# Kernel optimization log

Hardware: AMD Instinct MI355X
Metric: run time of the kernel (lower is better)

The kernel has to match this reference:

```python
import jax, jax.numpy as jnp
import numpy as np

N_CHANNELS = 1024
N_HEADS = 16
BLOCK_SIZE = 2048
BATCH = 4
SEQ = 2048


def setup_inputs() -> dict:
    key = jax.random.key(0)
    k_x, k_wqkv, k_wproj = jax.random.split(key, 3)
    x = jax.random.normal(k_x, (BATCH, SEQ, N_CHANNELS), dtype=jnp.float32)
    # torch nn.Linear: y = x @ W.T + b, W shape [out, in], init normal(std=0.02)
    W_qkv = jax.random.normal(k_wqkv, (3 * N_CHANNELS, N_CHANNELS), dtype=jnp.float32) * 0.02
    b_qkv = jnp.zeros((3 * N_CHANNELS,), dtype=jnp.float32)
    W_proj = jax.random.normal(k_wproj, (N_CHANNELS, N_CHANNELS), dtype=jnp.float32) * 0.02
    b_proj = jnp.zeros((N_CHANNELS,), dtype=jnp.float32)
    return {"x": x, "W_qkv": W_qkv, "b_qkv": b_qkv, "W_proj": W_proj, "b_proj": b_proj}


def reference(x, W_qkv, b_qkv, W_proj, b_proj):
    bs, n, n_channels = x.shape
    n_heads = N_HEADS
    head_dim = n_channels // n_heads
    scale = head_dim ** (-0.5)

    qkv = x @ W_qkv.T + b_qkv                              # [b, n, 3C]
    qkv = qkv.reshape(bs, n, 3, n_heads, head_dim)
    q, k, v = qkv[:, :, 0], qkv[:, :, 1], qkv[:, :, 2]     # [b, n, h, d]

    logits = jnp.einsum('bthc,bshc->bhts', q, k) * scale   # [b, h, t, s]
    # causal mask: log(tril(ones)) = 0 below diagonal, -inf above
    causal = jnp.tril(jnp.ones((n, n), dtype=bool))
    logits = jnp.where(causal[None, None], logits, -jnp.inf)
    attn = jax.nn.softmax(logits, axis=-1)

    output = jnp.einsum('bhts,bshc->bthc', attn, v)        # [b, t, h, d]
    output = output.reshape(bs, n, n_channels)
    output = output @ W_proj.T + b_proj
    return output
```

## Files before the change

### kernel.cpp

```cpp
#include <hip/hip_runtime.h>
#include <hip/hip_bf16.h>
#include <stdint.h>

#define BATCH 4
#define SEQ   2048
#define NC    1024
#define NH    16
#define HD    64
#define NT    16

typedef __bf16 bf16x8 __attribute__((ext_vector_type(8)));
typedef __bf16 bf16x4 __attribute__((ext_vector_type(4)));
typedef float  f32x4  __attribute__((ext_vector_type(4)));

#define DEV __device__ __forceinline__

DEV unsigned short f2bf(float f) {
    union { float f; unsigned u; } v; v.f = f;
    unsigned r = (v.u + 0x7fffu + ((v.u >> 16) & 1u)) >> 16;
    return (unsigned short)r;
}

DEV float fast_exp2(float x) {
#if __has_builtin(__builtin_amdgcn_exp2f)
    return __builtin_amdgcn_exp2f(x);
#else
    return exp2f(x);
#endif
}

#define GLDS16(gsrc, ldst)                                                           \
    __builtin_amdgcn_global_load_lds(                                                \
        (const __attribute__((address_space(1))) unsigned int*)(gsrc),               \
        (__attribute__((address_space(3))) unsigned int*)(ldst), 16, 0, 0)

__global__ void cvt_kernel(const float* __restrict__ in, unsigned short* __restrict__ out, int n4) {
    int i = blockIdx.x * 256 + threadIdx.x;
    if (i >= n4) return;
    float4 v = reinterpret_cast<const float4*>(in)[i];
    ushort4 o;
    o.x = f2bf(v.x); o.y = f2bf(v.y); o.z = f2bf(v.z); o.w = f2bf(v.w);
    reinterpret_cast<ushort4*>(out)[i] = o;
}

template <bool BF16_OUT>
__global__ __launch_bounds__(256, 2) void gemm_bt_kernel(
    const unsigned short* __restrict__ A,
    const unsigned short* __restrict__ W,
    const float* __restrict__ bias,
    void* __restrict__ Cout,
    int M, int N, int K, int scale_n, float scale)
{
    __shared__ __align__(16) char Alds[128 * 128];
    __shared__ __align__(16) char Blds[128 * 128];

    const int tid = threadIdx.x;
    const int w = tid >> 6, l = tid & 63, g = l >> 4, lr = l & 15;
    const int nt = N >> 7;
    const int mtile = blockIdx.x / nt, ntile = blockIdx.x % nt;
    const int m0 = mtile << 7, n0 = ntile << 7;
    const int wr = (w >> 1) << 6, wc = (w & 1) << 6;

    f32x4 acc[4][4] = {};

    for (int kt = 0; kt < K; kt += 64) {
        if (kt) __syncthreads();
#pragma unroll
        for (int i = 0; i < 4; ++i) {
            const int issue = (i << 2) + w;
            const int row = (issue << 3) + (l >> 3);
            const int chunk = (l & 7) ^ (row & 7);
            GLDS16((const char*)(A + (size_t)(m0 + row) * K + kt) + (chunk << 4),
                   Alds + (issue << 10));
        }
#pragma unroll
        for (int i = 0; i < 4; ++i) {
            const int issue = (i << 2) + w;
            const int row = (issue << 3) + (l >> 3);
            const int chunk = (l & 7) ^ (row & 7);
            GLDS16((const char*)(W + (size_t)(n0 + row) * K + kt) + (chunk << 4),
                   Blds + (issue << 10));
        }
        __syncthreads();

#pragma unroll
        for (int kb = 0; kb < 2; ++kb) {
            bf16x8 af[4], bfr[4];
#pragma unroll
            for (int mf = 0; mf < 4; ++mf) {
                const int row = wr + (mf << 4) + lr;
                const int chunk = ((kb << 2) + g) ^ (row & 7);
                af[mf] = *reinterpret_cast<const bf16x8*>(Alds + row * 128 + (chunk << 4));
            }
#pragma unroll
            for (int nf = 0; nf < 4; ++nf) {
                const int row = wc + (nf << 4) + lr;
                const int chunk = ((kb << 2) + g) ^ (row & 7);
                bfr[nf] = *reinterpret_cast<const bf16x8*>(Blds + row * 128 + (chunk << 4));
            }
#pragma unroll
            for (int mf = 0; mf < 4; ++mf)
#pragma unroll
                for (int nf = 0; nf < 4; ++nf)
                    acc[mf][nf] = __builtin_amdgcn_mfma_f32_16x16x32_bf16(
                        af[mf], bfr[nf], acc[mf][nf], 0, 0, 0);
        }
    }

#pragma unroll
    for (int mf = 0; mf < 4; ++mf) {
#pragma unroll
        for (int nf = 0; nf < 4; ++nf) {
            const int n = n0 + wc + (nf << 4) + lr;
            const float bscale = (n < scale_n) ? scale : 1.0f;
            const float bv = bias[n];
#pragma unroll
            for (int r = 0; r < 4; ++r) {
                const int m = m0 + wr + (mf << 4) + (g << 2) + r;
                float v2 = (acc[mf][nf][r] + bv) * bscale;
                if (BF16_OUT)
                    ((unsigned short*)Cout)[(size_t)m * N + n] = f2bf(v2);
                else
                    ((float*)Cout)[(size_t)m * N + n] = v2;
            }
        }
    }
}

__global__ __launch_bounds__(256, 2) void attn_kernel(
    const unsigned short* __restrict__ qkv,
    unsigned short* __restrict__ ctx)
{
    __shared__ __align__(16) char Klds[2][8192];
    __shared__ __align__(16) char Vt[2][64 * 144];
    __shared__ __align__(16) char Pl[4][32 * 144];

    const int tid = threadIdx.x;
    const int w = tid >> 6, l = tid & 63, g = l >> 4, lr = l & 15;
    const int p = blockIdx.x, h = blockIdx.y, b = blockIdx.z;
    const unsigned short* base = qkv + (size_t)b * SEQ * 3072 + h * 64;
    char* Pw = Pl[w];

    const int vkey0 = (tid >> 5) << 3;
    const int vd0   = (tid & 31) << 1;
    const unsigned short* vbase = base + 2048 + (size_t)vkey0 * 3072 + vd0;

    for (int pass = 0; pass < 2; ++pass) {
        const int qt = pass ? (NT - 1 - p) : p;
        const int q0 = (qt << 7) + (w << 5);
        const int ntiles = (qt + 1) << 1;

        bf16x8 qfr[2][2];
#pragma unroll
        for (int qi = 0; qi < 2; ++qi)
#pragma unroll
            for (int kb = 0; kb < 2; ++kb)
                qfr[qi][kb] = *reinterpret_cast<const bf16x8*>(
                    base + (size_t)(q0 + (qi << 4) + lr) * 3072 + (kb << 5) + (g << 3));

        f32x4 acc[2][4] = {};
        float mrun[2] = {-INFINITY, -INFINITY};
        float lrun[2] = {0.f, 0.f};

        uint32_t vreg[8];

#pragma unroll
        for (int i = 0; i < 8; ++i)
            vreg[i] = *reinterpret_cast<const uint32_t*>(vbase + (size_t)i * 3072);
#pragma unroll
        for (int i = 0; i < 2; ++i) {
            const int issue = (i << 2) + w;
            const int row = (issue << 3) + (l >> 3);
            const int chunk = (l & 7) ^ (row & 7);
            GLDS16((const char*)(base + 1024 + (size_t)row * 3072) + (chunk << 4),
                   Klds[0] + (issue << 10));
        }
        {
            uint4 a, bq;
            a.x = (vreg[0] & 0xffffu) | (vreg[1] << 16);
            a.y = (vreg[2] & 0xffffu) | (vreg[3] << 16);
            a.z = (vreg[4] & 0xffffu) | (vreg[5] << 16);
            a.w = (vreg[6] & 0xffffu) | (vreg[7] << 16);
            bq.x = (vreg[0] >> 16) | (vreg[1] & 0xffff0000u);
            bq.y = (vreg[2] >> 16) | (vreg[3] & 0xffff0000u);
            bq.z = (vreg[4] >> 16) | (vreg[5] & 0xffff0000u);
            bq.w = (vreg[6] >> 16) | (vreg[7] & 0xffff0000u);
            *reinterpret_cast<uint4*>(Vt[0] + vd0 * 144 + vkey0 * 2) = a;
            *reinterpret_cast<uint4*>(Vt[0] + (vd0 + 1) * 144 + vkey0 * 2) = bq;
        }
        __syncthreads();

        for (int t = 0; t < ntiles; ++t) {
            const int cur = t & 1;
            const int kv0 = t << 6;
            const bool pf_ = (t + 1 < ntiles);

            if (pf_) {
                const int kv1 = kv0 + 64;
#pragma unroll
                for (int i = 0; i < 8; ++i)
                    vreg[i] = *reinterpret_cast<const uint32_t*>(
                        vbase + (size_t)(kv1 + i) * 3072);
#pragma unroll
                for (int i = 0; i < 2; ++i) {
                    const int issue = (i << 2) + w;
                    const int row = (issue << 3) + (l >> 3);
                    const int chunk = (l & 7) ^ (row & 7);
                    GLDS16((const char*)(base + 1024 + (size_t)(kv1 + row) * 3072) + (chunk << 4),
                           Klds[cur ^ 1] + (issue << 10));
                }
            }

            if (kv0 <= q0 + 31) {
                f32x4 st[4][2] = {};
#pragma unroll
                for (int kb = 0; kb < 2; ++kb) {
                    bf16x8 kfr[4];
#pragma unroll
                    for (int kf = 0; kf < 4; ++kf) {
                        const int row = (kf << 4) + lr;
                        const int chunk = ((kb << 2) + g) ^ (row & 7);
                        kfr[kf] = *reinterpret_cast<const bf16x8*>(
                            Klds[cur] + row * 128 + (chunk << 4));
                    }
#pragma unroll
                    for (int kf = 0; kf < 4; ++kf)
#pragma unroll
                        for (int qi = 0; qi < 2; ++qi)
                            st[kf][qi] = __builtin_amdgcn_mfma_f32_16x16x32_bf16(
                                kfr[kf], qfr[qi][kb], st[kf][qi], 0, 0, 0);
                }
#pragma unroll
                for (int qi = 0; qi < 2; ++qi) {
                    const int qg = q0 + (qi << 4) + lr;
                    if (kv0 + 63 > qg) {
#pragma unroll
                        for (int kf = 0; kf < 4; ++kf)
#pragma unroll
                            for (int r = 0; r < 4; ++r) {
                                const int key = kv0 + (kf << 4) + (g << 2) + r;
                                if (key > qg) st[kf][qi][r] = -INFINITY;
                            }
                    }
                    float mt = -INFINITY;
#pragma unroll
                    for (int kf = 0; kf < 4; ++kf)
#pragma unroll
                        for (int r = 0; r < 4; ++r) mt = fmaxf(mt, st[kf][qi][r]);
                    mt = fmaxf(mt, __shfl_xor(mt, 16));
                    mt = fmaxf(mt, __shfl_xor(mt, 32));
                    const float mnew = fmaxf(mrun[qi], mt);
                    const float corr = fast_exp2(mrun[qi] - mnew);
                    mrun[qi] = mnew;
                    float rs = 0.f;
#pragma unroll
                    for (int kf = 0; kf < 4; ++kf) {
                        float p0 = fast_exp2(st[kf][qi][0] - mnew);
                        float p1 = fast_exp2(st[kf][qi][1] - mnew);
                        float p2 = fast_exp2(st[kf][qi][2] - mnew);
                        float p3 = fast_exp2(st[kf][qi][3] - mnew);
                        rs += (p0 + p1) + (p2 + p3);
                        bf16x4 pv = {(__bf16)p0, (__bf16)p1, (__bf16)p2, (__bf16)p3};
                        *reinterpret_cast<bf16x4*>(
                            Pw + (qi * 16 + lr) * 144 + (((kf << 4) + (g << 2)) << 1)) = pv;
                    }
                    rs += __shfl_xor(rs, 16);
                    rs += __shfl_xor(rs, 32);
                    lrun[qi] = lrun[qi] * corr + rs;
                    float cr[4];
#pragma unroll
                    for (int r = 0; r < 4; ++r) cr[r] = __shfl(corr, (l & 48) | ((g << 2) + r));
#pragma unroll
                    for (int df = 0; df < 4; ++df)
#pragma unroll
                        for (int r = 0; r < 4; ++r) acc[qi][df][r] *= cr[r];
                }
#pragma unroll
                for (int kb = 0; kb < 2; ++kb) {
                    bf16x8 pfv[2], vf[4];
#pragma unroll
                    for (int qi = 0; qi < 2; ++qi)
                        pfv[qi] = *reinterpret_cast<const bf16x8*>(
                            Pw + (qi * 16 + lr) * 144 + (((kb << 5) + (g << 3)) << 1));
#pragma unroll
                    for (int df = 0; df < 4; ++df)
                        vf[df] = *reinterpret_cast<const bf16x8*>(
                            Vt[cur] + ((df << 4) + lr) * 144 + (((kb << 5) + (g << 3)) << 1));
#pragma unroll
                    for (int qi = 0; qi < 2; ++qi)
#pragma unroll
                        for (int df = 0; df < 4; ++df)
                            acc[qi][df] = __builtin_amdgcn_mfma_f32_16x16x32_bf16(
                                pfv[qi], vf[df], acc[qi][df], 0, 0, 0);
                }
            }

            if (pf_) {
                uint4 a, bq;
                a.x = (vreg[0] & 0xffffu) | (vreg[1] << 16);
                a.y = (vreg[2] & 0xffffu) | (vreg[3] << 16);
                a.z = (vreg[4] & 0xffffu) | (vreg[5] << 16);
                a.w = (vreg[6] & 0xffffu) | (vreg[7] << 16);
                bq.x = (vreg[0] >> 16) | (vreg[1] & 0xffff0000u);
                bq.y = (vreg[2] >> 16) | (vreg[3] & 0xffff0000u);
                bq.z = (vreg[4] >> 16) | (vreg[5] & 0xffff0000u);
                bq.w = (vreg[6] >> 16) | (vreg[7] & 0xffff0000u);
                char* vt = Vt[cur ^ 1];
                *reinterpret_cast<uint4*>(vt + vd0 * 144 + vkey0 * 2) = a;
                *reinterpret_cast<uint4*>(vt + (vd0 + 1) * 144 + vkey0 * 2) = bq;
                __syncthreads();
            }
        }

#pragma unroll
        for (int qi = 0; qi < 2; ++qi) {
            const float li = 1.0f / lrun[qi];
            float lr4[4];
#pragma unroll
            for (int r = 0; r < 4; ++r) lr4[r] = __shfl(li, (l & 48) | ((g << 2) + r));
#pragma unroll
            for (int df = 0; df < 4; ++df)
#pragma unroll
                for (int r = 0; r < 4; ++r) {
                    const int qg = q0 + (qi << 4) + (g << 2) + r;
                    const int dd = (df << 4) + lr;
                    ctx[(size_t)(b * SEQ + qg) * NC + h * HD + dd] =
                        f2bf(acc[qi][df][r] * lr4[r]);
                }
        }
    }
}

extern "C" void kernel_launch(void* const* d_in, const int* in_sizes, int n_in,
                              void* d_out, int out_size, void* d_ws, size_t ws_size,
                              hipStream_t stream) {
    const float* x     = (const float*)d_in[0];
    const float* Wqkv  = (const float*)d_in[1];
    const float* bqkv  = (const float*)d_in[2];
    const float* Wproj = (const float*)d_in[3];
    const float* bproj = (const float*)d_in[4];
    float* out = (float*)d_out;

    const int M = BATCH * SEQ;
    unsigned short* ws = (unsigned short*)d_ws;
    unsigned short* xb     = ws;
    unsigned short* wqkvb  = xb + (size_t)M * NC;
    unsigned short* wprojb = wqkvb + (size_t)3 * NC * NC;
    unsigned short* qkvb   = wprojb + (size_t)NC * NC;
    unsigned short* ctxb   = qkvb + (size_t)M * 3 * NC;

    {
        int n4 = M * NC / 4;
        cvt_kernel<<<(n4 + 255) / 256, 256, 0, stream>>>(x, xb, n4);
    }
    {
        int n4 = 3 * NC * NC / 4;
        cvt_kernel<<<(n4 + 255) / 256, 256, 0, stream>>>(Wqkv, wqkvb, n4);
    }
    {
        int n4 = NC * NC / 4;
        cvt_kernel<<<(n4 + 255) / 256, 256, 0, stream>>>(Wproj, wprojb, n4);
    }

    gemm_bt_kernel<true><<<(M / 128) * (3 * NC / 128), 256, 0, stream>>>(
        xb, wqkvb, bqkv, qkvb, M, 3 * NC, NC, NC, 0.18033688011112042f);

    attn_kernel<<<dim3(SEQ / 256, NH, BATCH), 256, 0, stream>>>(qkvb, ctxb);

    gemm_bt_kernel<false><<<(M / 128) * (NC / 128), 256, 0, stream>>>(
        ctxb, wprojb, bproj, out, M, NC, NC, 0, 1.0f);
}
```

Baseline: 184.1 us.

## Remap blocks across XCDs, lazy softmax rescale, transpose PV MFMA output

Remaps block indices in both GEMM and attention kernels so that consecutive logical tiles land on the same XCD (a stride-8 swizzle), aiming at better L2 locality. Adds a lazy online-softmax rescale that only updates the running max and rescales the accumulator when some row's max grows by more than a threshold. Swaps the PV MFMA operand order so accumulator rows align with query lanes, which removes the corr/denominator shuffles, and skips the causal mask check per 16-row subtile. The lazy rescale lets the exponent base lag the true max, which risks larger intermediate values, and the epilogue store pattern changes.

```diff
diff --git a/kernel.cpp b/kernel.cpp
--- a/kernel.cpp
+++ b/kernel.cpp
@@ -57,7 +57,9 @@
     const int tid = threadIdx.x;
     const int w = tid >> 6, l = tid & 63, g = l >> 4, lr = l & 15;
     const int nt = N >> 7;
-    const int mtile = blockIdx.x / nt, ntile = blockIdx.x % nt;
+    const int cpx = gridDim.x >> 3;
+    const int bid = (blockIdx.x & 7) * cpx + (blockIdx.x >> 3);
+    const int mtile = bid / nt, ntile = bid % nt;
     const int m0 = mtile << 7, n0 = ntile << 7;
     const int wr = (w >> 1) << 6, wc = (w & 1) << 6;
 
@@ -137,7 +139,9 @@
 
     const int tid = threadIdx.x;
     const int w = tid >> 6, l = tid & 63, g = l >> 4, lr = l & 15;
-    const int p = blockIdx.x, h = blockIdx.y, b = blockIdx.z;
+    const int cpx = gridDim.x >> 3;
+    const int bid = (blockIdx.x & 7) * cpx + (blockIdx.x >> 3);
+    const int p = bid & 7, h = (bid >> 3) & 15, b = bid >> 7;
     const unsigned short* base = qkv + (size_t)b * SEQ * 3072 + h * 64;
     char* Pw = Pl[w];
 
@@ -232,8 +236,8 @@
                 }
 #pragma unroll
                 for (int qi = 0; qi < 2; ++qi) {
-                    const int qg = q0 + (qi << 4) + lr;
-                    if (kv0 + 63 > qg) {
+                    if (kv0 + 63 > q0 + (qi << 4)) {
+                        const int qg = q0 + (qi << 4) + lr;
 #pragma unroll
                         for (int kf = 0; kf < 4; ++kf)
 #pragma unroll
@@ -249,16 +253,23 @@
                         for (int r = 0; r < 4; ++r) mt = fmaxf(mt, st[kf][qi][r]);
                     mt = fmaxf(mt, __shfl_xor(mt, 16));
                     mt = fmaxf(mt, __shfl_xor(mt, 32));
-                    const float mnew = fmaxf(mrun[qi], mt);
-                    const float corr = fast_exp2(mrun[qi] - mnew);
-                    mrun[qi] = mnew;
+                    if (__any(mt > mrun[qi] + 8.0f)) {
+                        const float mnew = fmaxf(mrun[qi], mt);
+                        const float corr = fast_exp2(mrun[qi] - mnew);
+                        mrun[qi] = mnew;
+                        lrun[qi] *= corr;
+#pragma unroll
+                        for (int df = 0; df < 4; ++df)
+#pragma unroll
+                            for (int r = 0; r < 4; ++r) acc[qi][df][r] *= corr;
+                    }
                     float rs = 0.f;
 #pragma unroll
                     for (int kf = 0; kf < 4; ++kf) {
-                        float p0 = fast_exp2(st[kf][qi][0] - mnew);
-                        float p1 = fast_exp2(st[kf][qi][1] - mnew);
-                        float p2 = fast_exp2(st[kf][qi][2] - mnew);
-                        float p3 = fast_exp2(st[kf][qi][3] - mnew);
+                        float p0 = fast_exp2(st[kf][qi][0] - mrun[qi]);
+                        float p1 = fast_exp2(st[kf][qi][1] - mrun[qi]);
+                        float p2 = fast_exp2(st[kf][qi][2] - mrun[qi]);
+                        float p3 = fast_exp2(st[kf][qi][3] - mrun[qi]);
                         rs += (p0 + p1) + (p2 + p3);
                         bf16x4 pv = {(__bf16)p0, (__bf16)p1, (__bf16)p2, (__bf16)p3};
                         *reinterpret_cast<bf16x4*>(
@@ -266,14 +277,7 @@
                     }
                     rs += __shfl_xor(rs, 16);
                     rs += __shfl_xor(rs, 32);
-                    lrun[qi] = lrun[qi] * corr + rs;
-                    float cr[4];
-#pragma unroll
-                    for (int r = 0; r < 4; ++r) cr[r] = __shfl(corr, (l & 48) | ((g << 2) + r));
-#pragma unroll
-                    for (int df = 0; df < 4; ++df)
-#pragma unroll
-                        for (int r = 0; r < 4; ++r) acc[qi][df][r] *= cr[r];
+                    lrun[qi] += rs;
                 }
 #pragma unroll
                 for (int kb = 0; kb < 2; ++kb) {
@@ -291,7 +295,7 @@
 #pragma unroll
                         for (int df = 0; df < 4; ++df)
                             acc[qi][df] = __builtin_amdgcn_mfma_f32_16x16x32_bf16(
-                                pfv[qi], vf[df], acc[qi][df], 0, 0, 0);
+                                vf[df], pfv[qi], acc[qi][df], 0, 0, 0);
                 }
             }
 
@@ -315,18 +319,13 @@
 #pragma unroll
         for (int qi = 0; qi < 2; ++qi) {
             const float li = 1.0f / lrun[qi];
-            float lr4[4];
-#pragma unroll
-            for (int r = 0; r < 4; ++r) lr4[r] = __shfl(li, (l & 48) | ((g << 2) + r));
+            const int q = q0 + (qi << 4) + lr;
+            unsigned short* op = ctx + (size_t)(b * SEQ + q) * NC + h * HD;
 #pragma unroll
             for (int df = 0; df < 4; ++df)
 #pragma unroll
-                for (int r = 0; r < 4; ++r) {
-                    const int qg = q0 + (qi << 4) + (g << 2) + r;
-                    const int dd = (df << 4) + lr;
-                    ctx[(size_t)(b * SEQ + qg) * NC + h * HD + dd] =
-                        f2bf(acc[qi][df][r] * lr4[r]);
-                }
+                for (int r = 0; r < 4; ++r)
+                    op[(df << 4) + (g << 2) + r] = f2bf(acc[qi][df][r] * li);
         }
     }
 }
@@ -365,7 +364,7 @@
     gemm_bt_kernel<true><<<(M / 128) * (3 * NC / 128), 256, 0, stream>>>(
         xb, wqkvb, bqkv, qkvb, M, 3 * NC, NC, NC, 0.18033688011112042f);
 
-    attn_kernel<<<dim3(SEQ / 256, NH, BATCH), 256, 0, stream>>>(qkvb, ctxb);
+    attn_kernel<<<(SEQ / 256) * NH * BATCH, 256, 0, stream>>>(qkvb, ctxb);
 
     gemm_bt_kernel<false><<<(M / 128) * (NC / 128), 256, 0, stream>>>(
         ctxb, wprojb, bproj, out, M, NC, NC, 0, 1.0f);
```

New measurement: 173.3 us. -5.9%, faster.
